# Optimization experiments

Measured on AMD Instinct MI355X. Metric: run time of the kernel, lower is better.

Reference implementation:

```python
import jax, jax.numpy as jnp
import numpy as np

TIME_STEP = 0.1  # matches module-level time_step in the torch source
STEPS = 65536


def setup_inputs() -> dict:
    key = jax.random.key(0)
    k1, k2 = jax.random.split(key)
    x = jax.random.normal(k1, (12,), dtype=jnp.float32)          # initial state [pos(6), vel(6)]
    actions = jax.random.normal(k2, (STEPS, 6), dtype=jnp.float32)  # learned per-step accelerations
    return {"x": x, "actions": actions}


def reference(x, actions):
    dt = jnp.float32(TIME_STEP)
    half_dt2 = jnp.float32(0.5) * dt * dt

    def step(state, a):
        # state: [12] = [pos(6), vel(6)]; a: [6]
        pos = state[:6] + state[6:] * dt + half_dt2 * a
        vel = state[6:] + dt * a
        new_state = jnp.concatenate([pos, vel])
        return new_state, new_state

    _, states = jax.lax.scan(step, x, actions)  # states: [steps, 12]
    return (states, actions)
```

## Files before the change

kernel.cpp:

```cpp
#include <hip/hip_runtime.h>


#define STEPS    65536
#define NCH      6
#define NB       256
#define CHUNK    (STEPS / NB)
#define PER_LANE (CHUNK / 64)
#define BLK      (NCH * 64)

__global__ __launch_bounds__(BLK) void k_partial(const float* __restrict__ act,
                                                 double* __restrict__ bsum) {
    const int b    = blockIdx.x;
    const int c    = threadIdx.x >> 6;
    const int lane = threadIdx.x & 63;
    const int t0   = b * CHUNK + lane * PER_LANE;

    double sA = 0.0, sW = 0.0;
#pragma unroll
    for (int k = 0; k < PER_LANE; ++k) {
        const int   t = t0 + k;
        const float a = act[t * NCH + c];
        sA += (double)a;
        sW += (double)t * (double)a;
    }
#pragma unroll
    for (int off = 32; off > 0; off >>= 1) {
        sA += __shfl_down(sA, off, 64);
        sW += __shfl_down(sW, off, 64);
    }
    if (lane == 0) {
        bsum[(b * NCH + c) * 2 + 0] = sA;
        bsum[(b * NCH + c) * 2 + 1] = sW;
    }
}

__global__ __launch_bounds__(BLK) void k_final(const float* __restrict__ act,
                                               const float* __restrict__ x,
                                               const double* __restrict__ bsum,
                                               float* __restrict__ out) {
    const int b    = blockIdx.x;
    const int c    = threadIdx.x >> 6;
    const int lane = threadIdx.x & 63;

    double offA = 0.0, offW = 0.0;
    {
        double vA = 0.0, vW = 0.0;
#pragma unroll
        for (int j = 0; j < NB / 64; ++j) {
            const int l = lane * (NB / 64) + j;
            if (l < b) {
                vA += bsum[(l * NCH + c) * 2 + 0];
                vW += bsum[(l * NCH + c) * 2 + 1];
            }
        }
#pragma unroll
        for (int off = 32; off > 0; off >>= 1) {
            vA += __shfl_down(vA, off, 64);
            vW += __shfl_down(vW, off, 64);
        }
        offA = __shfl(vA, 0, 64);
        offW = __shfl(vW, 0, 64);
    }

    const int t0 = b * CHUNK + lane * PER_LANE;
    float av[PER_LANE];
    double sA = 0.0, sW = 0.0;
#pragma unroll
    for (int k = 0; k < PER_LANE; ++k) {
        const int   t = t0 + k;
        const float a = act[t * NCH + c];
        av[k] = a;
        sA += (double)a;
        sW += (double)t * (double)a;
    }

    double iA = sA, iW = sW;
#pragma unroll
    for (int off = 1; off < 64; off <<= 1) {
        const double uA = __shfl_up(iA, off, 64);
        const double uW = __shfl_up(iW, off, 64);
        if (lane >= off) { iA += uA; iW += uW; }
    }
    double runA = offA + iA - sA;
    double runW = offW + iW - sW;

    const double dt  = (double)0.1f;
    const double dt2 = dt * dt;
    const double p0  = (double)x[c];
    const double v0  = (double)x[6 + c];

#pragma unroll
    for (int k = 0; k < PER_LANE; ++k) {
        const int   t = t0 + k;
        const float a = av[k];
        runA += (double)a;
        runW += (double)t * (double)a;
        const double vel = v0 + dt * runA;
        const double pos = p0 + dt * (double)(t + 1) * v0
                         + dt2 * (((double)t + 0.5) * runA - runW);
        out[t * 12 + c]              = (float)pos;
        out[t * 12 + 6 + c]          = (float)vel;
        out[STEPS * 12 + t * NCH + c] = a;
    }
}

extern "C" void kernel_launch(void* const* d_in, const int* in_sizes, int n_in,
                              void* d_out, int out_size, void* d_ws, size_t ws_size,
                              hipStream_t stream) {
    const float* x       = (const float*)d_in[0];
    const float* actions = (const float*)d_in[1];
    float*       out     = (float*)d_out;
    double*      bsum    = (double*)d_ws;

    hipLaunchKernelGGL(k_partial, dim3(NB), dim3(BLK), 0, stream, actions, bsum);
    hipLaunchKernelGGL(k_final,   dim3(NB), dim3(BLK), 0, stream, actions, x, bsum, out);
}
```

Baseline: 65.47 us.

## Stage actions and outputs through LDS for coalesced float4 loads and stores

Both kernels now load each block's action chunk with coalesced float4 reads into shared memory, and the final kernel writes the state outputs via a shared-memory tile flushed as float4 stores. Lane-to-timestep mapping becomes interleaved, so the scan is done as four 64-wide wave scans with carried offsets instead of per-lane serial chunks. The actions copy moves into the first kernel. This targets strided scattered global accesses at the cost of LDS traffic, extra barriers and more shuffle scans.

```diff
diff --git a/kernel.cpp b/kernel.cpp
--- a/kernel.cpp
+++ b/kernel.cpp
@@ -1,27 +1,33 @@
 #include <hip/hip_runtime.h>
 
 
-#define STEPS    65536
-#define NCH      6
-#define NB       256
-#define CHUNK    (STEPS / NB)
-#define PER_LANE (CHUNK / 64)
-#define BLK      (NCH * 64)
+#define STEPS   65536
+#define NCH     6
+#define STATE   12
+#define NB      256
+#define CHUNK   (STEPS / NB)
+#define BLK     (NCH * 64)
+#define ACT_OFF (STEPS * STATE)
 
-__global__ __launch_bounds__(BLK) void k_partial(const float* __restrict__ act,
+__global__ __launch_bounds__(BLK) void k_partial(const float4* __restrict__ act4,
+                                                 float4* __restrict__ outact4,
                                                  double* __restrict__ bsum) {
-    const int b    = blockIdx.x;
-    const int c    = threadIdx.x >> 6;
-    const int lane = threadIdx.x & 63;
-    const int t0   = b * CHUNK + lane * PER_LANE;
+    __shared__ float sIn[CHUNK * NCH];
+    const int b = blockIdx.x, tid = threadIdx.x;
 
+    float4 v = act4[b * (CHUNK * NCH / 4) + tid];
+    outact4[b * (CHUNK * NCH / 4) + tid] = v;
+    ((float4*)sIn)[tid] = v;
+    __syncthreads();
+
+    const int c = tid >> 6, lane = tid & 63;
     double sA = 0.0, sW = 0.0;
 #pragma unroll
-    for (int k = 0; k < PER_LANE; ++k) {
-        const int   t = t0 + k;
-        const float a = act[t * NCH + c];
+    for (int k = 0; k < 4; ++k) {
+        const int   tl = k * 64 + lane;
+        const float a  = sIn[tl * NCH + c];
         sA += (double)a;
-        sW += (double)t * (double)a;
+        sW += (double)(b * CHUNK + tl) * (double)a;
     }
 #pragma unroll
     for (int off = 32; off > 0; off >>= 1) {
@@ -34,23 +40,28 @@
     }
 }
 
-__global__ __launch_bounds__(BLK) void k_final(const float* __restrict__ act,
+__global__ __launch_bounds__(BLK) void k_final(const float4* __restrict__ act4,
                                                const float* __restrict__ x,
                                                const double* __restrict__ bsum,
-                                               float* __restrict__ out) {
-    const int b    = blockIdx.x;
-    const int c    = threadIdx.x >> 6;
-    const int lane = threadIdx.x & 63;
+                                               float4* __restrict__ out4) {
+    __shared__ float sIn[CHUNK * NCH];
+    __shared__ float sOut[CHUNK * STATE];
+    const int b = blockIdx.x, tid = threadIdx.x;
 
-    double offA = 0.0, offW = 0.0;
+    ((float4*)sIn)[tid] = act4[b * (CHUNK * NCH / 4) + tid];
+    __syncthreads();
+
+    const int c = tid >> 6, lane = tid & 63;
+
+    double offA, offW;
     {
         double vA = 0.0, vW = 0.0;
 #pragma unroll
-        for (int j = 0; j < NB / 64; ++j) {
-            const int l = lane * (NB / 64) + j;
-            if (l < b) {
-                vA += bsum[(l * NCH + c) * 2 + 0];
-                vW += bsum[(l * NCH + c) * 2 + 1];
+        for (int k = 0; k < 4; ++k) {
+            const int idx = k * 64 + lane;
+            if (idx < b) {
+                vA += bsum[(idx * NCH + c) * 2 + 0];
+                vW += bsum[(idx * NCH + c) * 2 + 1];
             }
         }
 #pragma unroll
@@ -62,46 +73,40 @@
         offW = __shfl(vW, 0, 64);
     }
 
-    const int t0 = b * CHUNK + lane * PER_LANE;
-    float av[PER_LANE];
-    double sA = 0.0, sW = 0.0;
-#pragma unroll
-    for (int k = 0; k < PER_LANE; ++k) {
-        const int   t = t0 + k;
-        const float a = act[t * NCH + c];
-        av[k] = a;
-        sA += (double)a;
-        sW += (double)t * (double)a;
-    }
-
-    double iA = sA, iW = sW;
-#pragma unroll
-    for (int off = 1; off < 64; off <<= 1) {
-        const double uA = __shfl_up(iA, off, 64);
-        const double uW = __shfl_up(iW, off, 64);
-        if (lane >= off) { iA += uA; iW += uW; }
-    }
-    double runA = offA + iA - sA;
-    double runW = offW + iW - sW;
-
     const double dt  = (double)0.1f;
     const double dt2 = dt * dt;
     const double p0  = (double)x[c];
-    const double v0  = (double)x[6 + c];
+    const double v0  = (double)x[NCH + c];
 
+    double accA = offA, accW = offW;
 #pragma unroll
-    for (int k = 0; k < PER_LANE; ++k) {
-        const int   t = t0 + k;
-        const float a = av[k];
-        runA += (double)a;
-        runW += (double)t * (double)a;
+    for (int k = 0; k < 4; ++k) {
+        const int   tl = k * 64 + lane;
+        const int   t  = b * CHUNK + tl;
+        const float a  = sIn[tl * NCH + c];
+        double iA = (double)a;
+        double iW = (double)t * (double)a;
+#pragma unroll
+        for (int off = 1; off < 64; off <<= 1) {
+            const double uA = __shfl_up(iA, off, 64);
+            const double uW = __shfl_up(iW, off, 64);
+            if (lane >= off) { iA += uA; iW += uW; }
+        }
+        const double runA = accA + iA;
+        const double runW = accW + iW;
         const double vel = v0 + dt * runA;
         const double pos = p0 + dt * (double)(t + 1) * v0
                          + dt2 * (((double)t + 0.5) * runA - runW);
-        out[t * 12 + c]              = (float)pos;
-        out[t * 12 + 6 + c]          = (float)vel;
-        out[STEPS * 12 + t * NCH + c] = a;
+        sOut[tl * STATE + c]       = (float)pos;
+        sOut[tl * STATE + NCH + c] = (float)vel;
+        accA += __shfl(iA, 63, 64);
+        accW += __shfl(iW, 63, 64);
     }
+    __syncthreads();
+
+    const float4* so4 = (const float4*)sOut;
+    out4[b * (CHUNK * STATE / 4) + tid]       = so4[tid];
+    out4[b * (CHUNK * STATE / 4) + BLK + tid] = so4[BLK + tid];
 }
 
 extern "C" void kernel_launch(void* const* d_in, const int* in_sizes, int n_in,
@@ -112,6 +117,8 @@
     float*       out     = (float*)d_out;
     double*      bsum    = (double*)d_ws;
 
-    hipLaunchKernelGGL(k_partial, dim3(NB), dim3(BLK), 0, stream, actions, bsum);
-    hipLaunchKernelGGL(k_final,   dim3(NB), dim3(BLK), 0, stream, actions, x, bsum, out);
+    hipLaunchKernelGGL(k_partial, dim3(NB), dim3(BLK), 0, stream,
+                       (const float4*)actions, (float4*)(out + ACT_OFF), bsum);
+    hipLaunchKernelGGL(k_final, dim3(NB), dim3(BLK), 0, stream,
+                       (const float4*)actions, x, bsum, (float4*)out);
 }
```

New measurement: 62.46 us. 4.6% less time.
